# Kernel tuning notes

Measured on AMD Instinct MI355X. Metric: run time of the kernel, lower is better.

The kernel has to match this reference:

```python
import jax, jax.numpy as jnp
import numpy as np

B, G, L = 2048, 16384, 16


def setup_inputs() -> dict:
    key = jax.random.key(0)
    k1, k2, k3, k4 = jax.random.split(key, 4)
    return {
        "alpha_mu": jax.random.normal(k1, (B, L), dtype=jnp.float32),
        "alpha_var": jax.random.uniform(k2, (B, L), dtype=jnp.float32),
        "phi_mu": jax.random.normal(k3, (G, L), dtype=jnp.float32),
        "phi_var": jax.random.uniform(k4, (G, L), dtype=jnp.float32),
    }


def reference(alpha_mu, alpha_var, phi_mu, phi_var):
    # Moment matching for the product of independent Gaussians, summed over L:
    #   mean[b,g] = sum_l a_mu[b,l] * p_mu[g,l]
    #   var[b,g]  = sum_l a_var*p_mu^2 + p_var*a_mu^2 + a_var*p_var
    # Expressed as four [B,L]x[L,G] GEMMs instead of a [B,G,L] broadcast,
    # matching the original math exactly while avoiding the huge intermediate.
    pred_mean = jnp.einsum("bl,gl->bg", alpha_mu, phi_mu)
    pred_var = (
        jnp.einsum("bl,gl->bg", alpha_var, phi_mu * phi_mu)
        + jnp.einsum("bl,gl->bg", alpha_mu * alpha_mu, phi_var)
        + jnp.einsum("bl,gl->bg", alpha_var, phi_var)
    )
    return pred_mean, pred_var
```

## Files before the change

### kernel.cpp

```cpp
#include <hip/hip_runtime.h>


constexpr int L   = 16;
constexpr int RG  = 2;
constexpr int BT  = 64;
constexpr int TPB = 256;

typedef float v2f __attribute__((ext_vector_type(2)));

__global__ __launch_bounds__(TPB) void svgp_pod_kernel(
    const float* __restrict__ a_mu, const float* __restrict__ a_var,
    const float* __restrict__ p_mu, const float* __restrict__ p_var,
    float* __restrict__ out_mean, float* __restrict__ out_var,
    int B, int G)
{
    const int g0 = (blockIdx.x * TPB + threadIdx.x) * RG;
    const int b0 = blockIdx.y * BT;

    float pm[RG][L], pv[RG][L], q1[RG][L];
#pragma unroll
    for (int r = 0; r < RG; ++r) {
        const float4* pm4 = reinterpret_cast<const float4*>(p_mu + (long long)(g0 + r) * L);
        const float4* pv4 = reinterpret_cast<const float4*>(p_var + (long long)(g0 + r) * L);
#pragma unroll
        for (int c = 0; c < L / 4; ++c) {
            float4 m = pm4[c], v = pv4[c];
            pm[r][4*c+0] = m.x; pm[r][4*c+1] = m.y; pm[r][4*c+2] = m.z; pm[r][4*c+3] = m.w;
            pv[r][4*c+0] = v.x; pv[r][4*c+1] = v.y; pv[r][4*c+2] = v.z; pv[r][4*c+3] = v.w;
        }
#pragma unroll
        for (int l = 0; l < L; ++l) q1[r][l] = fmaf(pm[r][l], pm[r][l], pv[r][l]);
    }

    for (int i = 0; i < BT; ++i) {
        const int b = b0 + i;
        const float4* am4 = reinterpret_cast<const float4*>(a_mu + (long long)b * L);
        const float4* av4 = reinterpret_cast<const float4*>(a_var + (long long)b * L);
        float am[L], av[L];
#pragma unroll
        for (int c = 0; c < L / 4; ++c) {
            float4 m = am4[c], v = av4[c];
            am[4*c+0] = m.x; am[4*c+1] = m.y; am[4*c+2] = m.z; am[4*c+3] = m.w;
            av[4*c+0] = v.x; av[4*c+1] = v.y; av[4*c+2] = v.z; av[4*c+3] = v.w;
        }

        float mean[RG] = {0.f, 0.f}, var[RG] = {0.f, 0.f};
#pragma unroll
        for (int l = 0; l < L; ++l) {
            const float am2 = am[l] * am[l];
#pragma unroll
            for (int r = 0; r < RG; ++r) {
                mean[r] = fmaf(am[l], pm[r][l], mean[r]);
                var[r]  = fmaf(av[l], q1[r][l], var[r]);
                var[r]  = fmaf(am2,   pv[r][l], var[r]);
            }
        }

        const int off = b * G + g0;
        v2f mo = {mean[0], mean[1]};
        v2f vo = {var[0],  var[1]};
        *reinterpret_cast<v2f*>(out_mean + off) = mo;
        *reinterpret_cast<v2f*>(out_var  + off) = vo;
    }
}

extern "C" void kernel_launch(void* const* d_in, const int* in_sizes, int n_in,
                              void* d_out, int out_size, void* d_ws, size_t ws_size,
                              hipStream_t stream) {
    const float* a_mu  = (const float*)d_in[0];
    const float* a_var = (const float*)d_in[1];
    const float* p_mu  = (const float*)d_in[2];
    const float* p_var = (const float*)d_in[3];

    const int B = in_sizes[0] / L;
    const int G = in_sizes[2] / L;

    float* out_mean = (float*)d_out;
    float* out_var  = out_mean + (long long)B * G;

    dim3 grid((unsigned)(G / (TPB * RG)), (unsigned)(B / BT));
    svgp_pod_kernel<<<grid, TPB, 0, stream>>>(a_mu, a_var, p_mu, p_var,
                                              out_mean, out_var, B, G);
}
```

Measured before the change: 324.2 us.

## Stage alpha tile in LDS and use packed v2f FMAs across g pair

The block's 64-row alpha tile (mean, squared mean, variance) is loaded cooperatively into shared memory once, instead of every thread issuing its own global loads per row. The two g rows per thread are packed into float2 vectors so the inner FMAs can map to packed-FP32 instructions, and a_mu squared is precomputed once per tile. The row loop is unrolled by two. This adds a barrier and LDS broadcast reads, and the kernel likely stays bound by output write bandwidth.

Result: faster. 275.8 us (-14.9%).

```diff
diff --git a/kernel.cpp b/kernel.cpp
--- a/kernel.cpp
+++ b/kernel.cpp
@@ -14,53 +14,77 @@
     float* __restrict__ out_mean, float* __restrict__ out_var,
     int B, int G)
 {
-    const int g0 = (blockIdx.x * TPB + threadIdx.x) * RG;
-    const int b0 = blockIdx.y * BT;
+    __shared__ float4 s_am [BT][L / 4];
+    __shared__ float4 s_am2[BT][L / 4];
+    __shared__ float4 s_av [BT][L / 4];
 
-    float pm[RG][L], pv[RG][L], q1[RG][L];
-#pragma unroll
-    for (int r = 0; r < RG; ++r) {
-        const float4* pm4 = reinterpret_cast<const float4*>(p_mu + (long long)(g0 + r) * L);
-        const float4* pv4 = reinterpret_cast<const float4*>(p_var + (long long)(g0 + r) * L);
+    const int tid = threadIdx.x;
+    const int g0  = (blockIdx.x * TPB + tid) * RG;
+    const int b0  = blockIdx.y * BT;
+
+    {
+        const int r = tid >> 2;
+        const int c = tid & 3;
+        const long long base = (long long)(b0 + r) * L + c * 4;
+        float4 m = *reinterpret_cast<const float4*>(a_mu + base);
+        float4 v = *reinterpret_cast<const float4*>(a_var + base);
+        s_am [r][c] = m;
+        s_am2[r][c] = make_float4(m.x * m.x, m.y * m.y, m.z * m.z, m.w * m.w);
+        s_av [r][c] = v;
+    }
+
+    v2f pm2[L], pv2[L], q12[L];
+    {
+        const float4* pm4 = reinterpret_cast<const float4*>(p_mu + (long long)g0 * L);
+        const float4* pv4 = reinterpret_cast<const float4*>(p_var + (long long)g0 * L);
+        float rmA[L], rmB[L], rvA[L], rvB[L];
 #pragma unroll
         for (int c = 0; c < L / 4; ++c) {
-            float4 m = pm4[c], v = pv4[c];
-            pm[r][4*c+0] = m.x; pm[r][4*c+1] = m.y; pm[r][4*c+2] = m.z; pm[r][4*c+3] = m.w;
-            pv[r][4*c+0] = v.x; pv[r][4*c+1] = v.y; pv[r][4*c+2] = v.z; pv[r][4*c+3] = v.w;
+            float4 xa = pm4[c], xb = pm4[c + 4];
+            float4 ua = pv4[c], ub = pv4[c + 4];
+            rmA[4*c+0] = xa.x; rmA[4*c+1] = xa.y; rmA[4*c+2] = xa.z; rmA[4*c+3] = xa.w;
+            rmB[4*c+0] = xb.x; rmB[4*c+1] = xb.y; rmB[4*c+2] = xb.z; rmB[4*c+3] = xb.w;
+            rvA[4*c+0] = ua.x; rvA[4*c+1] = ua.y; rvA[4*c+2] = ua.z; rvA[4*c+3] = ua.w;
+            rvB[4*c+0] = ub.x; rvB[4*c+1] = ub.y; rvB[4*c+2] = ub.z; rvB[4*c+3] = ub.w;
         }
 #pragma unroll
-        for (int l = 0; l < L; ++l) q1[r][l] = fmaf(pm[r][l], pm[r][l], pv[r][l]);
+        for (int l = 0; l < L; ++l) {
+            pm2[l] = (v2f){rmA[l], rmB[l]};
+            pv2[l] = (v2f){rvA[l], rvB[l]};
+            q12[l] = pm2[l] * pm2[l] + pv2[l];
+        }
     }
 
+    __syncthreads();
+
+#pragma unroll 2
     for (int i = 0; i < BT; ++i) {
-        const int b = b0 + i;
-        const float4* am4 = reinterpret_cast<const float4*>(a_mu + (long long)b * L);
-        const float4* av4 = reinterpret_cast<const float4*>(a_var + (long long)b * L);
-        float am[L], av[L];
+        v2f mean = {0.f, 0.f}, var = {0.f, 0.f};
 #pragma unroll
         for (int c = 0; c < L / 4; ++c) {
-            float4 m = am4[c], v = av4[c];
-            am[4*c+0] = m.x; am[4*c+1] = m.y; am[4*c+2] = m.z; am[4*c+3] = m.w;
-            av[4*c+0] = v.x; av[4*c+1] = v.y; av[4*c+2] = v.z; av[4*c+3] = v.w;
+            const float4 am  = s_am [i][c];
+            const float4 am2 = s_am2[i][c];
+            const float4 av  = s_av [i][c];
+#define POD_STEP(J, AM, AM2, AV)                               \
+            {                                                  \
+                const int l = 4 * c + (J);                     \
+                const v2f amv  = {(AM),  (AM)};                \
+                const v2f am2v = {(AM2), (AM2)};               \
+                const v2f avv  = {(AV),  (AV)};                \
+                mean = amv  * pm2[l] + mean;                   \
+                var  = avv  * q12[l] + var;                    \
+                var  = am2v * pv2[l] + var;                    \
+            }
+            POD_STEP(0, am.x, am2.x, av.x)
+            POD_STEP(1, am.y, am2.y, av.y)
+            POD_STEP(2, am.z, am2.z, av.z)
+            POD_STEP(3, am.w, am2.w, av.w)
+#undef POD_STEP
         }
 
-        float mean[RG] = {0.f, 0.f}, var[RG] = {0.f, 0.f};
-#pragma unroll
-        for (int l = 0; l < L; ++l) {
-            const float am2 = am[l] * am[l];
-#pragma unroll
-            for (int r = 0; r < RG; ++r) {
-                mean[r] = fmaf(am[l], pm[r][l], mean[r]);
-                var[r]  = fmaf(av[l], q1[r][l], var[r]);
-                var[r]  = fmaf(am2,   pv[r][l], var[r]);
-            }
-        }
-
-        const int off = b * G + g0;
-        v2f mo = {mean[0], mean[1]};
-        v2f vo = {var[0],  var[1]};
-        *reinterpret_cast<v2f*>(out_mean + off) = mo;
-        *reinterpret_cast<v2f*>(out_var  + off) = vo;
+        const int off = (b0 + i) * G + g0;
+        *reinterpret_cast<v2f*>(out_mean + off) = mean;
+        *reinterpret_cast<v2f*>(out_var  + off) = var;
     }
 }
 
```

## Stage alpha tile in LDS, widen per-thread G to 4 with packed vector FMAs

Applied to the files above, without the earlier changes.

Each thread now computes four G columns instead of two, and the math is laid out as 4-wide vector ops so the compiler can emit packed FP32 FMAs. The block's alpha tile is loaded once into shared memory rather than reloaded from global by every thread on each row. Output stores become 16-byte vectors. The cost is higher register pressure, and q1 is recomputed inside the inner loop rather than precomputed. The grid in the host launch still divides by TPB*RG, so with RG=4 it launches half as many blocks along G.

Result: faster. 280.6 us (-13.4%).

```diff
diff --git a/kernel.cpp b/kernel.cpp
--- a/kernel.cpp
+++ b/kernel.cpp
@@ -2,11 +2,11 @@
 
 
 constexpr int L   = 16;
-constexpr int RG  = 2;
+constexpr int RG  = 4;
 constexpr int BT  = 64;
 constexpr int TPB = 256;
 
-typedef float v2f __attribute__((ext_vector_type(2)));
+typedef float v4f __attribute__((ext_vector_type(4)));
 
 __global__ __launch_bounds__(TPB) void svgp_pod_kernel(
     const float* __restrict__ a_mu, const float* __restrict__ a_var,
@@ -14,53 +14,65 @@
     float* __restrict__ out_mean, float* __restrict__ out_var,
     int B, int G)
 {
-    const int g0 = (blockIdx.x * TPB + threadIdx.x) * RG;
-    const int b0 = blockIdx.y * BT;
+    __shared__ v4f s_am[BT][L / 4];
+    __shared__ v4f s_av[BT][L / 4];
 
-    float pm[RG][L], pv[RG][L], q1[RG][L];
+    const int tid = threadIdx.x;
+    const int g0  = (blockIdx.x * TPB + tid) * RG;
+    const int b0  = blockIdx.y * BT;
+
+    {
+        const int r = tid >> 2;
+        const int c = tid & 3;
+        const long long base = (long long)(b0 + r) * L + c * 4;
+        s_am[r][c] = *reinterpret_cast<const v4f*>(a_mu + base);
+        s_av[r][c] = *reinterpret_cast<const v4f*>(a_var + base);
+    }
+
+    v4f pmv[L], pvv[L];
 #pragma unroll
     for (int r = 0; r < RG; ++r) {
-        const float4* pm4 = reinterpret_cast<const float4*>(p_mu + (long long)(g0 + r) * L);
-        const float4* pv4 = reinterpret_cast<const float4*>(p_var + (long long)(g0 + r) * L);
+        const v4f* pm4 = reinterpret_cast<const v4f*>(p_mu + (long long)(g0 + r) * L);
+        const v4f* pv4 = reinterpret_cast<const v4f*>(p_var + (long long)(g0 + r) * L);
 #pragma unroll
         for (int c = 0; c < L / 4; ++c) {
-            float4 m = pm4[c], v = pv4[c];
-            pm[r][4*c+0] = m.x; pm[r][4*c+1] = m.y; pm[r][4*c+2] = m.z; pm[r][4*c+3] = m.w;
-            pv[r][4*c+0] = v.x; pv[r][4*c+1] = v.y; pv[r][4*c+2] = v.z; pv[r][4*c+3] = v.w;
+            v4f m = pm4[c], v = pv4[c];
+            pmv[4*c+0][r] = m.x; pmv[4*c+1][r] = m.y;
+            pmv[4*c+2][r] = m.z; pmv[4*c+3][r] = m.w;
+            pvv[4*c+0][r] = v.x; pvv[4*c+1][r] = v.y;
+            pvv[4*c+2][r] = v.z; pvv[4*c+3][r] = v.w;
         }
-#pragma unroll
-        for (int l = 0; l < L; ++l) q1[r][l] = fmaf(pm[r][l], pm[r][l], pv[r][l]);
     }
 
+    __syncthreads();
+
+#pragma unroll 2
     for (int i = 0; i < BT; ++i) {
-        const int b = b0 + i;
-        const float4* am4 = reinterpret_cast<const float4*>(a_mu + (long long)b * L);
-        const float4* av4 = reinterpret_cast<const float4*>(a_var + (long long)b * L);
-        float am[L], av[L];
+        v4f mean = {0.f, 0.f, 0.f, 0.f};
+        v4f var  = {0.f, 0.f, 0.f, 0.f};
 #pragma unroll
         for (int c = 0; c < L / 4; ++c) {
-            float4 m = am4[c], v = av4[c];
-            am[4*c+0] = m.x; am[4*c+1] = m.y; am[4*c+2] = m.z; am[4*c+3] = m.w;
-            av[4*c+0] = v.x; av[4*c+1] = v.y; av[4*c+2] = v.z; av[4*c+3] = v.w;
+            const v4f am  = s_am[i][c];
+            const v4f av  = s_av[i][c];
+            const v4f am2 = am * am;
+#define POD_STEP(J)                                                    \
+            {                                                          \
+                const int l = 4 * c + (J);                             \
+                const v4f q1   = pmv[l] * pmv[l] + pvv[l];             \
+                const v4f amv  = {am[J],  am[J],  am[J],  am[J]};      \
+                const v4f am2v = {am2[J], am2[J], am2[J], am2[J]};     \
+                const v4f avv  = {av[J],  av[J],  av[J],  av[J]};      \
+                mean = amv  * pmv[l] + mean;                           \
+                var  = avv  * q1     + var;                            \
+                var  = am2v * pvv[l] + var;                            \
+            }
+            POD_STEP(0) POD_STEP(1) POD_STEP(2) POD_STEP(3)
+#undef POD_STEP
         }
 
-        float mean[RG] = {0.f, 0.f}, var[RG] = {0.f, 0.f};
-#pragma unroll
-        for (int l = 0; l < L; ++l) {
-            const float am2 = am[l] * am[l];
-#pragma unroll
-            for (int r = 0; r < RG; ++r) {
-                mean[r] = fmaf(am[l], pm[r][l], mean[r]);
-                var[r]  = fmaf(av[l], q1[r][l], var[r]);
-                var[r]  = fmaf(am2,   pv[r][l], var[r]);
-            }
-        }
-
-        const int off = b * G + g0;
-        v2f mo = {mean[0], mean[1]};
-        v2f vo = {var[0],  var[1]};
-        *reinterpret_cast<v2f*>(out_mean + off) = mo;
-        *reinterpret_cast<v2f*>(out_var  + off) = vo;
+        const int off = (b0 + i) * G + g0;
+        *reinterpret_cast<v4f*>(out_mean + off) = mean;
+        *reinterpret_cast<v4f*>(out_var  + off) = var;
     }
 }
 
```
